# Performance work log

Measured on AMD Instinct MI355X. Metric: run time of the kernel, lower is better.

## Reference

```python
import jax, jax.numpy as jnp
import numpy as np

N = 100000      # nodes
E = 3200000     # edges (avg degree 32)
G = 2048        # graphs in batch
F_IN = 4        # node feature dim (hardcoded in GCN.__init__)
H = 64          # hidden_dim default


def setup_inputs() -> dict:
    key = jax.random.key(0)
    ks = jax.random.split(key, 9)
    x = jax.random.normal(ks[0], (N, F_IN), dtype=jnp.float32)
    edge_index = jax.random.randint(ks[1], (2, E), 0, N, dtype=jnp.int64)
    batch = jnp.sort(jax.random.randint(ks[2], (N,), 0, G, dtype=jnp.int64))
    # learned params (Glorot-ish scaling)
    W1 = jax.random.normal(ks[3], (F_IN, H), dtype=jnp.float32) * (1.0 / np.sqrt(F_IN))
    b1 = jnp.zeros((H,), jnp.float32)
    W2 = jax.random.normal(ks[4], (H, H), dtype=jnp.float32) * (1.0 / np.sqrt(H))
    b2 = jnp.zeros((H,), jnp.float32)
    Wlin = jax.random.normal(ks[5], (H, 1), dtype=jnp.float32) * (1.0 / np.sqrt(H))
    blin = jnp.zeros((1,), jnp.float32)
    return {"x": x, "edge_index": edge_index, "batch": batch,
            "W1": W1, "b1": b1, "W2": W2, "b2": b2, "Wlin": Wlin, "blin": blin}


def _gcn_conv(x, W, b, src, dst, n):
    # PyG GCNConv: add self-loops, symmetric normalization D^-1/2 A_hat D^-1/2,
    # x' = x @ W, out[dst] += norm * x'[src], plus bias.
    xw = x @ W                                            # [N, H]
    deg = jnp.zeros((n,), xw.dtype).at[dst].add(1.0) + 1.0  # in-degree incl. self-loop
    dinv = jax.lax.rsqrt(deg)                             # deg^{-1/2}
    coef = (dinv[src] * dinv[dst])[:, None]               # [E, 1]
    agg = jax.ops.segment_sum(xw[src] * coef, dst, num_segments=n)  # neighbor msgs
    out = agg + xw * (1.0 / deg)[:, None]                 # self-loop contribution
    return out + b


def _global_mean_pool(x, batch, g):
    sums = jax.ops.segment_sum(x, batch, num_segments=g)
    cnt = jax.ops.segment_sum(jnp.ones((x.shape[0],), x.dtype), batch, num_segments=g)
    return sums / jnp.maximum(cnt, 1.0)[:, None]


def reference(x, edge_index, batch, W1, b1, W2, b2, Wlin, blin):
    src, dst = edge_index[0], edge_index[1]
    h = jax.nn.relu(_gcn_conv(x, W1, b1, src, dst, N))
    h = jax.nn.relu(_gcn_conv(h, W2, b2, src, dst, N))
    p = _global_mean_pool(h, batch, G)                    # [G, H]
    return p @ Wlin + blin                                # [G, 1]
```

## Files before the change

kernel.cpp:

```cpp
#include <hip/hip_runtime.h>
#include <hip/hip_fp16.h>

#define NN 100000
#define NE 3200000
#define NG 2048
#define HD 64
#define BUKSZ 256
#define NBUK 391
#define NB 512
#define CHUNK 6250
#define CAP 9216



__global__ void init_k(int* __restrict__ bcur) {
    int t = blockIdx.x * blockDim.x + threadIdx.x;
    if (t <= NBUK) bcur[t] = t * CAP;
}


__global__ __launch_bounds__(512) void stageA_k(
        const int* __restrict__ src, const int* __restrict__ dst,
        int* __restrict__ bcur, unsigned int* __restrict__ edges2) {
    __shared__ int hist[NBUK];
    __shared__ int exb[NBUK + 1];
    __shared__ int cur[NBUK];
    __shared__ int obase[NBUK];
    __shared__ int sc[512];
    __shared__ unsigned int svals[CHUNK];
    __shared__ unsigned short sbuk[CHUNK];
    int b = blockIdx.x, t = threadIdx.x;
    int base = b * CHUNK;
    for (int i = t; i < NBUK; i += 512) hist[i] = 0;
    __syncthreads();
    for (int i = t; i < CHUNK; i += 512)
        atomicAdd(&hist[dst[base + i] >> 8], 1);
    __syncthreads();
    int v = (t < NBUK) ? hist[t] : 0;
    sc[t] = v;
    __syncthreads();
    for (int o = 1; o < 512; o <<= 1) {
        int u = (t >= o) ? sc[t - o] : 0;
        __syncthreads();
        sc[t] += u;
        __syncthreads();
    }
    if (t < NBUK) {
        int excl = sc[t] - v;
        exb[t] = excl;
        cur[t] = excl;
        obase[t] = v ? atomicAdd(&bcur[t], v) : 0;
    }
    if (t == 0) exb[NBUK] = CHUNK;
    __syncthreads();
    for (int i = t; i < CHUNK; i += 512) {
        int d = dst[base + i];
        int s = src[base + i];
        int bk = d >> 8;
        int pos = atomicAdd(&cur[bk], 1);
        svals[pos] = ((unsigned int)(d & 255) << 17) | (unsigned int)s;
        sbuk[pos] = (unsigned short)bk;
    }
    __syncthreads();
    for (int i = t; i < CHUNK; i += 512) {
        int lo = (int)sbuk[i];
        edges2[obase[lo] + (i - exb[lo])] = svals[i];
    }
}


__global__ __launch_bounds__(512) void build1_k(
        const int* __restrict__ bcur, const float4* __restrict__ x,
        unsigned int* __restrict__ edges2, int* __restrict__ row_beg,
        int* __restrict__ row_deg, float* __restrict__ dinv,
        float4* __restrict__ xs) {
    __shared__ unsigned int ebuf[CAP];
    __shared__ int deg[BUKSZ];
    __shared__ int sc[BUKSZ];
    __shared__ int cur[BUKSZ];
    int k = blockIdx.x, t = threadIdx.x;
    int base = k * CAP;
    int len = bcur[k] - base;
    if (t < BUKSZ) deg[t] = 0;
    __syncthreads();
    for (int i = t; i < len; i += 512) {
        unsigned int pv = edges2[base + i];
        ebuf[i] = pv;
        atomicAdd(&deg[pv >> 17], 1);
    }
    __syncthreads();
    int v = 0;
    if (t < BUKSZ) { v = deg[t]; sc[t] = v; }
    __syncthreads();
    for (int o = 1; o < BUKSZ; o <<= 1) {
        int u = 0;
        if (t < BUKSZ && t >= o) u = sc[t - o];
        __syncthreads();
        if (t < BUKSZ && t >= o) sc[t] += u;
        __syncthreads();
    }
    if (t < BUKSZ) {
        int excl = sc[t] - v;
        cur[t] = excl;
        int node = k * BUKSZ + t;
        if (node < NN) {
            row_beg[node] = base + excl;
            row_deg[node] = v;
            float di = rsqrtf((float)v + 1.0f);
            dinv[node] = di;
            float4 xv = x[node];
            xs[node] = make_float4(xv.x * di, xv.y * di, xv.z * di, xv.w * di);
        }
    }
    __syncthreads();
    for (int i = t; i < len; i += 512) {
        unsigned int pv = ebuf[i];
        int pos = atomicAdd(&cur[pv >> 17], 1);
        edges2[base + pos] = pv & 0x1FFFFu;
    }
}


__global__ __launch_bounds__(256) void g1f_k(
        const float4* __restrict__ xs, const unsigned int* __restrict__ csr,
        const int* __restrict__ row_beg, const int* __restrict__ row_deg,
        const float* __restrict__ dinv, const float* __restrict__ W1,
        const float* __restrict__ b1, __half* __restrict__ h1) {
    int wid = (blockIdx.x * blockDim.x + threadIdx.x) >> 6;
    int lane = threadIdx.x & 63;
    if (wid >= NN) return;
    int beg = row_beg[wid], deg = row_deg[wid];
    float sx = 0.f, sy = 0.f, sz = 0.f, sw = 0.f;
    for (int e = beg + lane; e < beg + deg; e += 64) {
        float4 w = xs[csr[e]];
        sx += w.x; sy += w.y; sz += w.z; sw += w.w;
    }
#pragma unroll
    for (int o = 1; o < 64; o <<= 1) {
        sx += __shfl_xor(sx, o);
        sy += __shfl_xor(sy, o);
        sz += __shfl_xor(sz, o);
        sw += __shfl_xor(sw, o);
    }
    float di = dinv[wid];
    float4 self = xs[wid];
    float ax = (sx + self.x) * di;
    float ay = (sy + self.y) * di;
    float az = (sz + self.z) * di;
    float aw = (sw + self.w) * di;
    float v = ax * W1[lane] + ay * W1[64 + lane] + az * W1[128 + lane] + aw * W1[192 + lane] + b1[lane];
    v = fmaxf(v, 0.f) * di;
    h1[(size_t)wid * HD + lane] = __float2half_rn(v);
}


union H8 { int4 i4; __half2 h2[4]; };

__global__ __launch_bounds__(256) void gather2_k(
        const __half* __restrict__ h1, const unsigned int* __restrict__ csr,
        const int* __restrict__ row_beg, const int* __restrict__ row_deg,
        __half* __restrict__ a2h) {
    __shared__ int sidx[4][64];
    int wv = threadIdx.x >> 6;
    int wid = (blockIdx.x * blockDim.x + threadIdx.x) >> 6;
    int lane = threadIdx.x & 63;
    if (wid >= NN) return;
    int half = lane >> 5;
    int g = (lane >> 3) & 3;
    int sub = lane & 7;
    int hg = half * 4 + g;
    int beg = row_beg[wid], deg = row_deg[wid];
    float accx[4] = {0.f, 0.f, 0.f, 0.f};
    float accy[4] = {0.f, 0.f, 0.f, 0.f};
    int done = 0;
    while (done < deg) {
        int chunk = deg - done;
        if (chunk > 64) chunk = 64;
        if (lane < chunk) sidx[wv][lane] = (int)csr[beg + done + lane];
        int kb = 0;
        for (; kb + 31 < chunk; kb += 32) {
            int e0 = sidx[wv][kb + hg];
            int e1 = sidx[wv][kb + hg + 8];
            int e2 = sidx[wv][kb + hg + 16];
            int e3 = sidx[wv][kb + hg + 24];
            H8 r0, r1, r2, r3;
            r0.i4 = *(const int4*)(h1 + (size_t)e0 * HD + sub * 8);
            r1.i4 = *(const int4*)(h1 + (size_t)e1 * HD + sub * 8);
            r2.i4 = *(const int4*)(h1 + (size_t)e2 * HD + sub * 8);
            r3.i4 = *(const int4*)(h1 + (size_t)e3 * HD + sub * 8);
#pragma unroll
            for (int j = 0; j < 4; ++j) {
                float2 f0 = __half22float2(r0.h2[j]);
                float2 f1 = __half22float2(r1.h2[j]);
                float2 f2 = __half22float2(r2.h2[j]);
                float2 f3 = __half22float2(r3.h2[j]);
                accx[j] += (f0.x + f1.x) + (f2.x + f3.x);
                accy[j] += (f0.y + f1.y) + (f2.y + f3.y);
            }
        }
        for (; kb + 7 < chunk; kb += 8) {
            int e0 = sidx[wv][kb + hg];
            H8 r0;
            r0.i4 = *(const int4*)(h1 + (size_t)e0 * HD + sub * 8);
#pragma unroll
            for (int j = 0; j < 4; ++j) {
                float2 f0 = __half22float2(r0.h2[j]);
                accx[j] += f0.x;
                accy[j] += f0.y;
            }
        }
        if (kb < chunk) {
            int e = kb + hg;
            if (e < chunk) {
                int e0 = sidx[wv][e];
                H8 r0;
                r0.i4 = *(const int4*)(h1 + (size_t)e0 * HD + sub * 8);
#pragma unroll
                for (int j = 0; j < 4; ++j) {
                    float2 f0 = __half22float2(r0.h2[j]);
                    accx[j] += f0.x;
                    accy[j] += f0.y;
                }
            }
        }
        done += chunk;
    }
#pragma unroll
    for (int j = 0; j < 4; ++j) {
        accx[j] += __shfl_xor(accx[j], 8);
        accy[j] += __shfl_xor(accy[j], 8);
        accx[j] += __shfl_xor(accx[j], 16);
        accy[j] += __shfl_xor(accy[j], 16);
        accx[j] += __shfl_xor(accx[j], 32);
        accy[j] += __shfl_xor(accy[j], 32);
    }
    if (half == 0 && g == 0) {
        H8 sv, o;
        sv.i4 = *(const int4*)(h1 + (size_t)wid * HD + sub * 8);
#pragma unroll
        for (int j = 0; j < 4; ++j) {
            float2 fs = __half22float2(sv.h2[j]);
            o.h2[j] = __floats2half2_rn(accx[j] + fs.x, accy[j] + fs.y);
        }
        ((int4*)a2h)[(size_t)wid * 8 + sub] = o.i4;
    }
}


__global__ __launch_bounds__(512) void combine2_pool_k(
        const __half* __restrict__ a2h, const float* __restrict__ W2,
        const float* __restrict__ b2, const float* __restrict__ dinv,
        const int* __restrict__ batch, float* __restrict__ pool) {
    __shared__ float w2s[HD * HD];
    __shared__ float as2[32][HD];
    __shared__ float vals[32][HD];
    __shared__ int   bt[32];
    int tid = threadIdx.x;
    int wave = tid >> 6, lane = tid & 63;
    int base = blockIdx.x * 32;
    for (int i = tid; i < HD * HD; i += 512) w2s[i] = W2[i];
    for (int i = tid; i < 32 * HD; i += 512)
        as2[i >> 6][i & 63] = __half2float(a2h[(size_t)base * HD + i]);
    if (tid < 32) bt[tid] = batch[base + tid];
    __syncthreads();
#pragma unroll
    for (int r = 0; r < 4; ++r) {
        int nl = wave * 4 + r;
        float s = 0.f;
#pragma unroll
        for (int k = 0; k < HD; ++k) s = fmaf(as2[nl][k], w2s[k * HD + lane], s);
        float v = fmaxf(fmaf(dinv[base + nl], s, b2[lane]), 0.f);
        vals[nl][lane] = v;
    }
    __syncthreads();
    if (wave == 0) {
        int g = bt[0];
        float acc = 0.f;
        for (int i = 0; i < 32; ++i) {
            int bg = bt[i];
            if (bg != g) { atomicAdd(&pool[g * HD + lane], acc); acc = 0.f; g = bg; }
            acc += vals[i][lane];
        }
        atomicAdd(&pool[g * HD + lane], acc);
    }
}

__device__ __forceinline__ int lb_dev(const int* __restrict__ b, int n, int key) {
    int lo = 0, hi = n;
    while (lo < hi) {
        int mid = (lo + hi) >> 1;
        if (b[mid] < key) lo = mid + 1; else hi = mid;
    }
    return lo;
}

__global__ void final_k(const float* __restrict__ pool, const int* __restrict__ batch,
                        const float* __restrict__ Wlin, const float* __restrict__ blin,
                        float* __restrict__ out) {
    int g = blockIdx.x;
    int lane = threadIdx.x;
    int lo = lb_dev(batch, NN, g);
    int hi = lb_dev(batch, NN, g + 1);
    float cnt = (float)(hi - lo);
    float v = pool[g * HD + lane] * Wlin[lane];
#pragma unroll
    for (int off = 32; off > 0; off >>= 1) v += __shfl_down(v, off);
    if (lane == 0) out[g] = v / fmaxf(cnt, 1.0f) + blin[0];
}


extern "C" void kernel_launch(void* const* d_in, const int* in_sizes, int n_in,
                              void* d_out, int out_size, void* d_ws, size_t ws_size,
                              hipStream_t stream) {
    const float* x    = (const float*)d_in[0];
    const int*   ei   = (const int*)d_in[1];
    const int*   bat  = (const int*)d_in[2];
    const float* W1   = (const float*)d_in[3];
    const float* b1   = (const float*)d_in[4];
    const float* W2   = (const float*)d_in[5];
    const float* b2   = (const float*)d_in[6];
    const float* Wlin = (const float*)d_in[7];
    const float* blin = (const float*)d_in[8];
    float* out = (float*)d_out;

    const int* src = ei;
    const int* dst = ei + NE;

    char* ws = (char*)d_ws;
    size_t off = 0;
    auto alloc = [&](size_t bytes) {
        char* p = ws + off;
        off += (bytes + 255) & ~(size_t)255;
        return p;
    };
    int*   bcur    = (int*)  alloc((NBUK + 1) * sizeof(int));
    int*   row_beg = (int*)  alloc(NN * sizeof(int));
    int*   row_deg = (int*)  alloc(NN * sizeof(int));
    float* dinv    = (float*)alloc(NN * sizeof(float));
    unsigned int* edges2 = (unsigned int*)alloc((size_t)NBUK * CAP * sizeof(unsigned int));
    float4* xs     = (float4*)alloc((size_t)NN * sizeof(float4));
    __half* h1     = (__half*)alloc((size_t)NN * HD * sizeof(__half));
    __half* a2h    = (__half*)alloc((size_t)NN * HD * sizeof(__half));
    float* pool    = (float*)alloc((size_t)NG * HD * sizeof(float));
    (void)ws_size; (void)n_in; (void)in_sizes; (void)out_size;

    const int BLK = 256;
    const int gW = (NN * 64 + BLK - 1) / BLK;

    init_k<<<(NBUK + 1 + 255) / 256, 256, 0, stream>>>(bcur);
    stageA_k<<<NB, 512, 0, stream>>>(src, dst, bcur, edges2);
    build1_k<<<NBUK, 512, 0, stream>>>(bcur, (const float4*)x, edges2,
                                       row_beg, row_deg, dinv, xs);

    g1f_k<<<gW, BLK, 0, stream>>>(xs, edges2, row_beg, row_deg, dinv, W1, b1, h1);

    gather2_k<<<gW, BLK, 0, stream>>>(h1, edges2, row_beg, row_deg, a2h);

    hipMemsetAsync(pool, 0, (size_t)NG * HD * sizeof(float), stream);
    combine2_pool_k<<<NN / 32, 512, 0, stream>>>(a2h, W2, b2, dinv, bat, pool);
    final_k<<<NG, 64, 0, stream>>>(pool, bat, Wlin, blin, out);
}
```

Before: 202.7 us.

## Rewrite combine2 pool kernel to use register-resident W2 and readlane broadcast

The combine kernel no longer stages W2, node activations and outputs in shared memory. Each lane now keeps one column of W2 in registers, each wave handles 8 nodes, and node features are broadcast across the wave with readlane, so the block-wide barriers and LDS traffic go away. Pooling is done per wave, with fewer nodes merged before each atomic. The cost is higher register pressure from the 64-entry W2 column, and every wave reloads W2 from global memory, which may cut occupancy and raise the number of atomics.

```diff
diff --git a/kernel.cpp b/kernel.cpp
--- a/kernel.cpp
+++ b/kernel.cpp
@@ -251,38 +251,44 @@
         const __half* __restrict__ a2h, const float* __restrict__ W2,
         const float* __restrict__ b2, const float* __restrict__ dinv,
         const int* __restrict__ batch, float* __restrict__ pool) {
-    __shared__ float w2s[HD * HD];
-    __shared__ float as2[32][HD];
-    __shared__ float vals[32][HD];
-    __shared__ int   bt[32];
     int tid = threadIdx.x;
     int wave = tid >> 6, lane = tid & 63;
-    int base = blockIdx.x * 32;
-    for (int i = tid; i < HD * HD; i += 512) w2s[i] = W2[i];
-    for (int i = tid; i < 32 * HD; i += 512)
-        as2[i >> 6][i & 63] = __half2float(a2h[(size_t)base * HD + i]);
-    if (tid < 32) bt[tid] = batch[base + tid];
-    __syncthreads();
-#pragma unroll
-    for (int r = 0; r < 4; ++r) {
-        int nl = wave * 4 + r;
-        float s = 0.f;
-#pragma unroll
-        for (int k = 0; k < HD; ++k) s = fmaf(as2[nl][k], w2s[k * HD + lane], s);
-        float v = fmaxf(fmaf(dinv[base + nl], s, b2[lane]), 0.f);
-        vals[nl][lane] = v;
-    }
-    __syncthreads();
-    if (wave == 0) {
-        int g = bt[0];
-        float acc = 0.f;
-        for (int i = 0; i < 32; ++i) {
-            int bg = bt[i];
-            if (bg != g) { atomicAdd(&pool[g * HD + lane], acc); acc = 0.f; g = bg; }
-            acc += vals[i][lane];
-        }
-        atomicAdd(&pool[g * HD + lane], acc);
-    }
+    int base = blockIdx.x * 64 + wave * 8;
+    float wcol[64];
+#pragma unroll
+    for (int k = 0; k < 64; ++k) wcol[k] = W2[k * HD + lane];
+    float bv = b2[lane];
+    float a[8];
+#pragma unroll
+    for (int i = 0; i < 8; ++i) {
+        int node = base + i;
+        a[i] = (node < NN) ? __half2float(a2h[(size_t)node * HD + lane]) : 0.f;
+    }
+    float s[8] = {0.f, 0.f, 0.f, 0.f, 0.f, 0.f, 0.f, 0.f};
+#pragma unroll
+    for (int k = 0; k < 64; ++k) {
+        float w = wcol[k];
+#pragma unroll
+        for (int i = 0; i < 8; ++i) {
+            float av = __int_as_float(__builtin_amdgcn_readlane(__float_as_int(a[i]), k));
+            s[i] = fmaf(av, w, s[i]);
+        }
+    }
+    int g = -1;
+    float acc = 0.f;
+#pragma unroll
+    for (int i = 0; i < 8; ++i) {
+        int node = base + i;
+        if (node >= NN) break;
+        float v = fmaxf(fmaf(dinv[node], s[i], bv), 0.f);
+        int bg = batch[node];
+        if (bg != g) {
+            if (g >= 0) atomicAdd(&pool[g * HD + lane], acc);
+            acc = 0.f; g = bg;
+        }
+        acc += v;
+    }
+    if (g >= 0) atomicAdd(&pool[g * HD + lane], acc);
 }
 
 __device__ __forceinline__ int lb_dev(const int* __restrict__ b, int n, int key) {
@@ -357,6 +363,6 @@
     gather2_k<<<gW, BLK, 0, stream>>>(h1, edges2, row_beg, row_deg, a2h);
 
     hipMemsetAsync(pool, 0, (size_t)NG * HD * sizeof(float), stream);
-    combine2_pool_k<<<NN / 32, 512, 0, stream>>>(a2h, W2, b2, dinv, bat, pool);
+    combine2_pool_k<<<(NN + 63) / 64, 512, 0, stream>>>(a2h, W2, b2, dinv, bat, pool);
     final_k<<<NG, 64, 0, stream>>>(pool, bat, Wlin, blin, out);
 }
```

After: 207.0 us. +2.1%, slower.
